# Performance work log

Hardware: AMD Instinct MI355X
Metric: run time of the kernel (lower is better)

## Reference

```python
import jax, jax.numpy as jnp
import numpy as np

B, S, D_IN, D_OUT, H = 2, 2048, 1024, 1024, 16
HD = D_OUT // H


def setup_inputs() -> dict:
    key = jax.random.key(0)
    ks = jax.random.split(key, 6)
    x = jax.random.normal(ks[0], (B, S, D_IN), jnp.float32)
    Wq = jax.random.normal(ks[1], (D_IN, D_OUT), jnp.float32) * 0.02
    Wk = jax.random.normal(ks[2], (D_IN, D_OUT), jnp.float32) * 0.02
    Wv = jax.random.normal(ks[3], (D_IN, D_OUT), jnp.float32) * 0.02
    Wo = jax.random.normal(ks[4], (D_OUT, D_OUT), jnp.float32) * 0.02
    bo = jax.random.normal(ks[5], (D_OUT,), jnp.float32) * 0.02
    return {"x": x, "Wq": Wq, "Wk": Wk, "Wv": Wv, "Wo": Wo, "bo": bo}


def reference(x, Wq, Wk, Wv, Wo, bo):
    b, s, _ = x.shape

    def to_heads(t):  # [b, s, d_out] -> [b, h, s, hd]
        return t.reshape(b, s, H, HD).transpose(0, 2, 1, 3)

    Q = to_heads(x @ Wq)
    K = to_heads(x @ Wk)
    V = to_heads(x @ Wv)

    scale = 1.0 / jnp.sqrt(jnp.asarray(HD, x.dtype))
    scores = jnp.einsum("bhqd,bhkd->bhqk", Q, K) * scale
    causal_mask = jnp.triu(jnp.ones((s, s), dtype=bool), k=1)  # True above diag
    scores = jnp.where(causal_mask, jnp.asarray(-1e6, scores.dtype), scores)
    weights = jax.nn.softmax(scores, axis=-1)  # dropout p=0.0 -> identity
    attn = jnp.einsum("bhqk,bhkd->bhqd", weights, V)  # [b, h, s, hd]
    # Faithful to source: reshape [b,h,s,hd] -> [b,s,d_out] WITHOUT head transpose-back
    attn = attn.reshape(b, s, D_OUT)
    return attn @ Wo + bo
```

## Files before the change

### kernel.cpp

```cpp
#include <hip/hip_runtime.h>
#include <stdint.h>


typedef unsigned short u16;
typedef __attribute__((ext_vector_type(8))) short bf16x8;
typedef __attribute__((ext_vector_type(4))) float f32x4;

#define MFMA_BF16(a, b, c) __builtin_amdgcn_mfma_f32_16x16x32_bf16((a), (b), (c), 0, 0, 0)
#define QSCALE 0.18033688011112042f

__device__ __forceinline__ u16 f2bf(float f) {
  union { float f; unsigned int u; } x; x.f = f;
  unsigned int r = x.u + 0x7fffu + ((x.u >> 16) & 1u);
  return (u16)(r >> 16);
}
__device__ __forceinline__ bf16x8 pack8(float4 a, float4 b) {
  bf16x8 r;
  r[0] = (short)f2bf(a.x); r[1] = (short)f2bf(a.y);
  r[2] = (short)f2bf(a.z); r[3] = (short)f2bf(a.w);
  r[4] = (short)f2bf(b.x); r[5] = (short)f2bf(b.y);
  r[6] = (short)f2bf(b.z); r[7] = (short)f2bf(b.w);
  return r;
}
__device__ __forceinline__ void gload_lds16(const u16* g, u16* l) {
  __builtin_amdgcn_global_load_lds((__attribute__((address_space(1))) void*)g,
                                   (__attribute__((address_space(3))) void*)l, 16, 0, 0);
}

template <int CPR>
__device__ __forceinline__ int sw_off(int r, int c) {
  return (r * CPR + (c ^ (r & (CPR - 1)))) * 8;
}

__global__ __launch_bounds__(256) void x_to_bf16(const float* __restrict__ x,
                                                 u16* __restrict__ xb) {
  const size_t i = ((size_t)blockIdx.x * 256 + threadIdx.x) * 8;
  const float4 a = *(const float4*)&x[i];
  const float4 b = *(const float4*)&x[i + 4];
  *(bf16x8*)&xb[i] = pack8(a, b);
}

__global__ void transpose_cols(const float* __restrict__ W0, const float* __restrict__ W1,
                               const float* __restrict__ W2, u16* __restrict__ T,
                               int h0, int hsx64) {
  __shared__ u16 t[32][33];
  const int j0 = blockIdx.x * 32;
  const int g = j0 / hsx64;
  const float* W = (g == 0) ? W0 : (g == 1) ? W1 : W2;
  const int wc0 = h0 * 64 + (j0 % hsx64);
  const int k0 = blockIdx.y * 32;
  t[threadIdx.y][threadIdx.x] =
      f2bf(W[(size_t)(k0 + threadIdx.y) * 1024 + wc0 + threadIdx.x]);
  __syncthreads();
  T[(size_t)(j0 + threadIdx.y) * 1024 + k0 + threadIdx.x] = t[threadIdx.x][threadIdx.y];
}

template <int MODE, int AF32>
__global__ __launch_bounds__(256, 2) void gemm_bt(
    const void* __restrict__ Av, const u16* __restrict__ BT,
    void* __restrict__ C0v, u16* __restrict__ C1, u16* __restrict__ C2,
    const float* __restrict__ bias, int M, int N, int K, int hs, int h0) {
  __shared__ __align__(16) u16 lsA[128 * 32];
  __shared__ __align__(16) u16 lsB[128 * 32];
  const int tid = threadIdx.x, lane = tid & 63, wv = tid >> 6;
  const int quad = lane >> 4, l16 = lane & 15;
  const int m0 = blockIdx.y * 128, n0 = blockIdx.x * 128;
  const int wm = (wv >> 1) * 64, wn = (wv & 1) * 64;
  const int hs64 = hs * 64;
  f32x4 acc[4][4] = {};

  for (int k0 = 0; k0 < K; k0 += 32) {
    if constexpr (AF32) {
      bf16x8 va[2], vb[2];
#pragma unroll
      for (int c = 0; c < 2; ++c) {
        const int P = c * 256 + tid, r = P >> 2, cc = P & 3;
        const float* Af = (const float*)Av;
        const float4 a0 = *(const float4*)&Af[(size_t)(m0 + r) * K + k0 + cc * 8];
        const float4 a1 = *(const float4*)&Af[(size_t)(m0 + r) * K + k0 + cc * 8 + 4];
        va[c] = pack8(a0, a1);
        vb[c] = *(const bf16x8*)&BT[(size_t)(n0 + r) * K + k0 + cc * 8];
      }
      __syncthreads();
#pragma unroll
      for (int c = 0; c < 2; ++c) {
        const int P = c * 256 + tid, r = P >> 2, cc = P & 3;
        *(bf16x8*)&lsA[sw_off<4>(r, cc)] = va[c];
        *(bf16x8*)&lsB[sw_off<4>(r, cc)] = vb[c];
      }
      __syncthreads();
    } else {
      __syncthreads();
#pragma unroll
      for (int c = 0; c < 2; ++c) {
        const int P = c * 256 + tid, r = P >> 2;
        const int gcol = ((P & 3) ^ (r & 3)) * 8;
        gload_lds16((const u16*)Av + (size_t)(m0 + r) * K + k0 + gcol,
                    &lsA[(size_t)(c * 256 + wv * 64) * 8]);
        gload_lds16(BT + (size_t)(n0 + r) * K + k0 + gcol,
                    &lsB[(size_t)(c * 256 + wv * 64) * 8]);
      }
      __syncthreads();
    }
    bf16x8 af[4], bfr[4];
#pragma unroll
    for (int i = 0; i < 4; ++i) af[i] = *(const bf16x8*)&lsA[sw_off<4>(wm + i * 16 + l16, quad)];
#pragma unroll
    for (int j = 0; j < 4; ++j) bfr[j] = *(const bf16x8*)&lsB[sw_off<4>(wn + j * 16 + l16, quad)];
#pragma unroll
    for (int i = 0; i < 4; ++i)
#pragma unroll
      for (int j = 0; j < 4; ++j) acc[i][j] = MFMA_BF16(af[i], bfr[j], acc[i][j]);
  }

#pragma unroll
  for (int i = 0; i < 4; ++i)
#pragma unroll
    for (int j = 0; j < 4; ++j) {
      const int n = n0 + wn + j * 16 + l16;
      float bv = 0.f;
      if constexpr (MODE == 1) bv = bias[n];
#pragma unroll
      for (int r = 0; r < 4; ++r) {
        const int m = m0 + wm + i * 16 + quad * 4 + r;
        if constexpr (MODE == 3) {
          const int b = m >> 11, s = m & 2047;
          if (n < hs64) {
            ((u16*)C0v)[((size_t)b * 2048 + s) * hs64 + n] = f2bf(acc[i][j][r] * QSCALE);
          } else if (n < 2 * hs64) {
            C1[((size_t)b * 2048 + s) * hs64 + (n - hs64)] = f2bf(acc[i][j][r]);
          } else {
            const int nn = n - 2 * hs64;
            C2[((size_t)(b * hs + (nn >> 6)) * 64 + (nn & 63)) * 2048 + s] =
                f2bf(acc[i][j][r]);
          }
        } else {
          const int b = (m >= hs * 128) ? 1 : 0;
          const int rp = m - b * hs * 128;
          ((float*)C0v)[(size_t)(b * 2048 + h0 * 128 + rp) * 1024 + n] =
              acc[i][j][r] + bv;
        }
      }
    }
}

__global__ __launch_bounds__(512, 2) void attn_fwd(
    const u16* __restrict__ Qsl, const u16* __restrict__ Ksl,
    const u16* __restrict__ VTsl, u16* __restrict__ A2sl, int hs) {
  __shared__ __align__(16) u16 lsK[2][128 * 64];
  __shared__ __align__(16) u16 lsV[2][64 * 128];
  __shared__ __align__(16) u16 lsP[8][16 * 36];
  const int tid = threadIdx.x, lane = tid & 63, wv = tid >> 6;
  const int quad = lane >> 4, l16 = lane & 15;
  const int bh = blockIdx.y;
  const int b = (bh >= hs) ? 1 : 0, hh = bh - b * hs;
  const int hs64 = hs * 64;
  const int wm = wv * 16;
  const u16* Qb = Qsl + (size_t)b * 2048 * hs64;
  const u16* Kb = Ksl + (size_t)b * 2048 * hs64;
  const u16* Vb = VTsl + (size_t)(b * hs + hh) * 64 * 2048;
  u16* A2b = A2sl + (size_t)(b * hs + hh) * 2048 * 64;
  u16* lsPw = &lsP[wv][0];

  bf16x8 ones;
#pragma unroll
  for (int i = 0; i < 8; ++i) ones[i] = (short)0x3F80;

  const int P0 = tid, P1 = 512 + tid;

  for (int half = 0; half < 2; ++half) {
    const int qt = (half == 0) ? (int)blockIdx.x : 15 - (int)blockIdx.x;
    const int q0 = qt * 128;

    bf16x8 qf[2];
#pragma unroll
    for (int ks = 0; ks < 2; ++ks)
      qf[ks] = *(const bf16x8*)&Qb[(size_t)(q0 + wm + l16) * hs64 + hh * 64 +
                                   ks * 32 + quad * 8];

    f32x4 acc_o[4] = {};
    f32x4 acc_l = {};

    bf16x8 vk0, vk1, vv0, vv1, nk0, nk1, nv0, nv1;
    vk0 = *(const bf16x8*)&Kb[(size_t)(P0 >> 3) * hs64 + hh * 64 + (P0 & 7) * 8];
    vk1 = *(const bf16x8*)&Kb[(size_t)(P1 >> 3) * hs64 + hh * 64 + (P1 & 7) * 8];
    vv0 = *(const bf16x8*)&Vb[(size_t)(P0 >> 4) * 2048 + (P0 & 15) * 8];
    vv1 = *(const bf16x8*)&Vb[(size_t)(P1 >> 4) * 2048 + (P1 & 15) * 8];

    for (int kt = 0; kt <= qt; ++kt) {
      const int k0 = kt * 128;
      const int buf = kt & 1;
      *(bf16x8*)&lsK[buf][sw_off<8>(P0 >> 3, P0 & 7)] = vk0;
      *(bf16x8*)&lsK[buf][sw_off<8>(P1 >> 3, P1 & 7)] = vk1;
      *(bf16x8*)&lsV[buf][sw_off<16>(P0 >> 4, P0 & 15)] = vv0;
      *(bf16x8*)&lsV[buf][sw_off<16>(P1 >> 4, P1 & 15)] = vv1;
      if (kt < qt) {
        const int k1 = k0 + 128;
        nk0 = *(const bf16x8*)&Kb[(size_t)(k1 + (P0 >> 3)) * hs64 + hh * 64 + (P0 & 7) * 8];
        nk1 = *(const bf16x8*)&Kb[(size_t)(k1 + (P1 >> 3)) * hs64 + hh * 64 + (P1 & 7) * 8];
        nv0 = *(const bf16x8*)&Vb[(size_t)(P0 >> 4) * 2048 + k1 + (P0 & 15) * 8];
        nv1 = *(const bf16x8*)&Vb[(size_t)(P1 >> 4) * 2048 + k1 + (P1 & 15) * 8];
      }
      __syncthreads();

      f32x4 accs[8] = {};
#pragma unroll
      for (int ks = 0; ks < 2; ++ks)
#pragma unroll
        for (int nj = 0; nj < 8; ++nj) {
          const bf16x8 kf =
              *(const bf16x8*)&lsK[buf][sw_off<8>(nj * 16 + l16, ks * 4 + quad)];
          accs[nj] = MFMA_BF16(qf[ks], kf, accs[nj]);
        }

      const bool diag = (kt == qt);
#pragma unroll
      for (int nj = 0; nj < 8; ++nj)
#pragma unroll
        for (int r = 0; r < 4; ++r) {
          float p = exp2f(accs[nj][r]);
          if (diag) {
            const int col = k0 + nj * 16 + l16;
            const int grow = q0 + wm + quad * 4 + r;
            p = (col > grow) ? 0.f : p;
          }
          accs[nj][r] = p;
        }

#pragma unroll
      for (int ks2 = 0; ks2 < 4; ++ks2) {
#pragma unroll
        for (int jj = 0; jj < 2; ++jj)
#pragma unroll
          for (int r = 0; r < 4; ++r) {
            union { float f; unsigned int u; } t;
            t.f = accs[ks2 * 2 + jj][r];
            lsPw[(quad * 4 + r) * 36 + jj * 16 + l16] = (u16)(t.u >> 16);
          }
        const bf16x8 pf = *(const bf16x8*)&lsPw[l16 * 36 + quad * 8];
        acc_l = MFMA_BF16(pf, ones, acc_l);
#pragma unroll
        for (int njo = 0; njo < 4; ++njo) {
          const bf16x8 vf =
              *(const bf16x8*)&lsV[buf][sw_off<16>(njo * 16 + l16, ks2 * 4 + quad)];
          acc_o[njo] = MFMA_BF16(pf, vf, acc_o[njo]);
        }
      }

      vk0 = nk0; vk1 = nk1; vv0 = nv0; vv1 = nv1;
    }

#pragma unroll
    for (int r = 0; r < 4; ++r) {
      const int q = q0 + wm + quad * 4 + r;
      const float inv = 1.0f / acc_l[r];
#pragma unroll
      for (int njo = 0; njo < 4; ++njo)
        A2b[(size_t)q * 64 + njo * 16 + l16] = f2bf(acc_o[njo][r] * inv);
    }
    __syncthreads();
  }
}

extern "C" void kernel_launch(void* const* d_in, const int* in_sizes, int n_in,
                              void* d_out, int out_size, void* d_ws, size_t ws_size,
                              hipStream_t stream) {
  (void)in_sizes; (void)n_in; (void)out_size;
  const float* x  = (const float*)d_in[0];
  const float* Wq = (const float*)d_in[1];
  const float* Wk = (const float*)d_in[2];
  const float* Wv = (const float*)d_in[3];
  const float* Wo = (const float*)d_in[4];
  const float* bo = (const float*)d_in[5];
  float* out = (float*)d_out;
  char* ws = (char*)d_ws;
  const size_t MB = 1024 * 1024;
  const size_t KB = 1024;

  int hs = 2;
  if      (ws_size >= 2 * MB + 16 * 2432 * KB) hs = 16;
  else if (ws_size >= 2 * MB +  8 * 2432 * KB) hs = 8;
  else if (ws_size >= 2 * MB +  4 * 2432 * KB) hs = 4;

  u16* WoT   = (u16*)(ws);
  u16* Ksl   = (u16*)(ws + 2 * MB);
  u16* VTsl  = (u16*)(ws + 2 * MB + (size_t)hs *  512 * KB);
  u16* A2sl  = (u16*)(ws + 2 * MB + (size_t)hs * 1024 * KB);
  u16* WT3sl = (u16*)(ws + 2 * MB + (size_t)hs * 1536 * KB);
  u16* Qsl   = (u16*)(ws + 2 * MB + (size_t)hs * 1920 * KB);

  transpose_cols<<<dim3(32, 32), dim3(32, 32), 0, stream>>>(Wo, Wo, Wo, WoT, 0, 1024);
  if (hs == 16) {
    u16* xb = A2sl;
    x_to_bf16<<<2048, 256, 0, stream>>>(x, xb);
    transpose_cols<<<dim3(96, 32), dim3(32, 32), 0, stream>>>(Wq, Wk, Wv, WT3sl, 0, 1024);
    gemm_bt<3, 0><<<dim3(24, 32), 256, 0, stream>>>(
        (const void*)xb, WT3sl, (void*)Qsl, Ksl, VTsl, nullptr, 4096, 3072, 1024, 16, 0);
    attn_fwd<<<dim3(8, 32), 512, 0, stream>>>(Qsl, Ksl, VTsl, A2sl, 16);
    gemm_bt<1, 0><<<dim3(8, 32), 256, 0, stream>>>(
        (const void*)A2sl, WoT, (void*)out, nullptr, nullptr, bo, 4096, 1024, 1024, 16, 0);
  } else {
    for (int h0 = 0; h0 < 16; h0 += hs) {
      transpose_cols<<<dim3(6 * hs, 32), dim3(32, 32), 0, stream>>>(Wq, Wk, Wv, WT3sl, h0, hs * 64);
      gemm_bt<3, 1><<<dim3((3 * hs) / 2, 32), 256, 0, stream>>>(
          (const void*)x, WT3sl, (void*)Qsl, Ksl, VTsl, nullptr, 4096, 3 * hs * 64, 1024, hs, h0);
      attn_fwd<<<dim3(8, 2 * hs), 512, 0, stream>>>(Qsl, Ksl, VTsl, A2sl, hs);
      gemm_bt<1, 0><<<dim3(8, 2 * hs), 256, 0, stream>>>(
          (const void*)A2sl, WoT, (void*)out, nullptr, nullptr, bo, 2 * hs * 128, 1024, 1024, hs, h0);
    }
  }
}
```

Before: 210.8 us.

## Split attention query tiles across two 256-thread blocks with XCD-aware block remap

The attention kernel now uses 256-thread blocks that each handle a 64-row half of a 128-row query tile, doubling the grid to a 1D launch of 16*2*hs blocks. Block indices are remapped so that consecutive work items (same batch-head) land on the same chiplet via a blockIdx&7 swizzle, which should improve L2 reuse of K/V. Each thread now loads four K/V chunks instead of two. This adds parallelism and occupancy, at the cost of each block reloading the full K/V tiles for half the query work, which doubles K/V traffic into LDS.

```diff
diff --git a/kernel.cpp b/kernel.cpp
--- a/kernel.cpp
+++ b/kernel.cpp
@@ -144,15 +144,21 @@
     }
 }
 
-__global__ __launch_bounds__(512, 2) void attn_fwd(
+__global__ __launch_bounds__(256, 2) void attn_fwd(
     const u16* __restrict__ Qsl, const u16* __restrict__ Ksl,
     const u16* __restrict__ VTsl, u16* __restrict__ A2sl, int hs) {
   __shared__ __align__(16) u16 lsK[2][128 * 64];
   __shared__ __align__(16) u16 lsV[2][64 * 128];
-  __shared__ __align__(16) u16 lsP[8][16 * 36];
+  __shared__ __align__(16) u16 lsP[4][16 * 36];
   const int tid = threadIdx.x, lane = tid & 63, wv = tid >> 6;
   const int quad = lane >> 4, l16 = lane & 15;
-  const int bh = blockIdx.y;
+
+  const int cpx = gridDim.x >> 3;
+  const int w = (blockIdx.x & 7) * cpx + (blockIdx.x >> 3);
+  const int bh = w >> 4;
+  const int bx = w & 15;
+  const int pairidx = bx >> 1, slice = bx & 1;
+
   const int b = (bh >= hs) ? 1 : 0, hh = bh - b * hs;
   const int hs64 = hs * 64;
   const int wm = wv * 16;
@@ -166,11 +172,13 @@
 #pragma unroll
   for (int i = 0; i < 8; ++i) ones[i] = (short)0x3F80;
 
-  const int P0 = tid, P1 = 512 + tid;
+  bf16x8 vk[4], vv[4], nk[4], nv[4];
+#pragma unroll
+  for (int c = 0; c < 4; ++c) { nk[c] = {}; nv[c] = {}; }
 
   for (int half = 0; half < 2; ++half) {
-    const int qt = (half == 0) ? (int)blockIdx.x : 15 - (int)blockIdx.x;
-    const int q0 = qt * 128;
+    const int qt = (half == 0) ? pairidx : 15 - pairidx;
+    const int q0 = qt * 128 + slice * 64;
 
     bf16x8 qf[2];
 #pragma unroll
@@ -181,25 +189,30 @@
     f32x4 acc_o[4] = {};
     f32x4 acc_l = {};
 
-    bf16x8 vk0, vk1, vv0, vv1, nk0, nk1, nv0, nv1;
-    vk0 = *(const bf16x8*)&Kb[(size_t)(P0 >> 3) * hs64 + hh * 64 + (P0 & 7) * 8];
-    vk1 = *(const bf16x8*)&Kb[(size_t)(P1 >> 3) * hs64 + hh * 64 + (P1 & 7) * 8];
-    vv0 = *(const bf16x8*)&Vb[(size_t)(P0 >> 4) * 2048 + (P0 & 15) * 8];
-    vv1 = *(const bf16x8*)&Vb[(size_t)(P1 >> 4) * 2048 + (P1 & 15) * 8];
+#pragma unroll
+    for (int c = 0; c < 4; ++c) {
+      const int P = c * 256 + tid;
+      vk[c] = *(const bf16x8*)&Kb[(size_t)(P >> 3) * hs64 + hh * 64 + (P & 7) * 8];
+      vv[c] = *(const bf16x8*)&Vb[(size_t)(P >> 4) * 2048 + (P & 15) * 8];
+    }
 
     for (int kt = 0; kt <= qt; ++kt) {
       const int k0 = kt * 128;
       const int buf = kt & 1;
-      *(bf16x8*)&lsK[buf][sw_off<8>(P0 >> 3, P0 & 7)] = vk0;
-      *(bf16x8*)&lsK[buf][sw_off<8>(P1 >> 3, P1 & 7)] = vk1;
-      *(bf16x8*)&lsV[buf][sw_off<16>(P0 >> 4, P0 & 15)] = vv0;
-      *(bf16x8*)&lsV[buf][sw_off<16>(P1 >> 4, P1 & 15)] = vv1;
+#pragma unroll
+      for (int c = 0; c < 4; ++c) {
+        const int P = c * 256 + tid;
+        *(bf16x8*)&lsK[buf][sw_off<8>(P >> 3, P & 7)] = vk[c];
+        *(bf16x8*)&lsV[buf][sw_off<16>(P >> 4, P & 15)] = vv[c];
+      }
       if (kt < qt) {
         const int k1 = k0 + 128;
-        nk0 = *(const bf16x8*)&Kb[(size_t)(k1 + (P0 >> 3)) * hs64 + hh * 64 + (P0 & 7) * 8];
-        nk1 = *(const bf16x8*)&Kb[(size_t)(k1 + (P1 >> 3)) * hs64 + hh * 64 + (P1 & 7) * 8];
-        nv0 = *(const bf16x8*)&Vb[(size_t)(P0 >> 4) * 2048 + k1 + (P0 & 15) * 8];
-        nv1 = *(const bf16x8*)&Vb[(size_t)(P1 >> 4) * 2048 + k1 + (P1 & 15) * 8];
+#pragma unroll
+        for (int c = 0; c < 4; ++c) {
+          const int P = c * 256 + tid;
+          nk[c] = *(const bf16x8*)&Kb[(size_t)(k1 + (P >> 3)) * hs64 + hh * 64 + (P & 7) * 8];
+          nv[c] = *(const bf16x8*)&Vb[(size_t)(P >> 4) * 2048 + k1 + (P & 15) * 8];
+        }
       }
       __syncthreads();
 
@@ -247,7 +260,8 @@
         }
       }
 
-      vk0 = nk0; vk1 = nk1; vv0 = nv0; vv1 = nv1;
+#pragma unroll
+      for (int c = 0; c < 4; ++c) { vk[c] = nk[c]; vv[c] = nv[c]; }
     }
 
 #pragma unroll
@@ -296,7 +310,7 @@
     transpose_cols<<<dim3(96, 32), dim3(32, 32), 0, stream>>>(Wq, Wk, Wv, WT3sl, 0, 1024);
     gemm_bt<3, 0><<<dim3(24, 32), 256, 0, stream>>>(
         (const void*)xb, WT3sl, (void*)Qsl, Ksl, VTsl, nullptr, 4096, 3072, 1024, 16, 0);
-    attn_fwd<<<dim3(8, 32), 512, 0, stream>>>(Qsl, Ksl, VTsl, A2sl, 16);
+    attn_fwd<<<dim3(512), 256, 0, stream>>>(Qsl, Ksl, VTsl, A2sl, 16);
     gemm_bt<1, 0><<<dim3(8, 32), 256, 0, stream>>>(
         (const void*)A2sl, WoT, (void*)out, nullptr, nullptr, bo, 4096, 1024, 1024, 16, 0);
   } else {
@@ -304,7 +318,7 @@
       transpose_cols<<<dim3(6 * hs, 32), dim3(32, 32), 0, stream>>>(Wq, Wk, Wv, WT3sl, h0, hs * 64);
       gemm_bt<3, 1><<<dim3((3 * hs) / 2, 32), 256, 0, stream>>>(
           (const void*)x, WT3sl, (void*)Qsl, Ksl, VTsl, nullptr, 4096, 3 * hs * 64, 1024, hs, h0);
-      attn_fwd<<<dim3(8, 2 * hs), 512, 0, stream>>>(Qsl, Ksl, VTsl, A2sl, hs);
+      attn_fwd<<<dim3(16 * 2 * hs), 256, 0, stream>>>(Qsl, Ksl, VTsl, A2sl, hs);
       gemm_bt<1, 0><<<dim3(8, 2 * hs), 256, 0, stream>>>(
           (const void*)A2sl, WoT, (void*)out, nullptr, nullptr, bo, 2 * hs * 128, 1024, 1024, hs, h0);
     }
```

New measurement: 209.0 us. About the same (-0.9%).
